# Optimization experiments

Measured on AMD Instinct MI355X. Metric: run time of the kernel, lower is better.

Reference implementation:

```python
import jax, jax.numpy as jnp
import numpy as np

NUM_HEADS = 4

def setup_inputs() -> dict:
    key = jax.random.key(0)
    ks = jax.random.split(key, 6)
    B, C, D, H, W = 2, 64, 16, 16, 16
    return {
        "x": jax.random.normal(ks[0], (B, C, D, H, W), dtype=jnp.float32),
        "tpm": jax.random.uniform(ks[1], (B, 1, D, H, W), dtype=jnp.float32),
        "qkv_w": jax.random.normal(ks[2], (3 * C, C), dtype=jnp.float32) * 0.05,
        "qkv_b": jax.random.normal(ks[3], (3 * C,), dtype=jnp.float32) * 0.02,
        "proj_w": jax.random.normal(ks[4], (C, C), dtype=jnp.float32) * 0.05,
        "proj_b": jax.random.normal(ks[5], (C,), dtype=jnp.float32) * 0.02,
        "temperature": jnp.ones((1,), dtype=jnp.float32),
    }


def reference(x, tpm, qkv_w, qkv_b, proj_w, proj_b, temperature):
    B, C, D, H, W = x.shape
    N = D * H * W
    nh = NUM_HEADS
    hd = C // nh
    scale = hd ** (-0.5)

    xf = x.reshape(B, C, N)
    # 1x1x1 Conv3d == per-voxel linear over channels
    qkv = jnp.einsum('oc,bcn->bon', qkv_w, xf) + qkv_b[:, None]  # (B,3C,N)
    qkv = qkv.reshape(B, 3, nh, hd, N)
    q, k, v = qkv[:, 0], qkv[:, 1], qkv[:, 2]  # each (B,nh,hd,N)

    temp = jnp.clip(temperature, 0.1, 2.0)[0]
    attn = jnp.einsum('bhdi,bhdj->bhij', q, k) * (scale * temp)  # (B,nh,N,N)

    tpm_c = jnp.clip(tpm, 0.01, 1.0).reshape(B, 1, N)
    tpm_inter = (tpm_c[:, :, :, None] + tpm_c[:, :, None, :]) * 0.5  # (B,1,N,N)
    attn = attn * tpm_inter
    attn = jax.nn.softmax(attn, axis=-1)  # dropout p=0.0 -> identity

    out = jnp.einsum('bhij,bhdj->bhdi', attn, v)  # (B,nh,hd,N)
    out = out.reshape(B, C, N)
    out = jnp.einsum('oc,bcn->bon', proj_w, out) + proj_b[:, None]
    return out.reshape(B, C, D, H, W)
```

## Files before the change

### kernel.cpp

```cpp
#include <hip/hip_runtime.h>
#include <hip/hip_bf16.h>
#include <math.h>

typedef __attribute__((ext_vector_type(8))) short bf16x8_t;
typedef __attribute__((ext_vector_type(4))) int i32x4_t;
typedef __attribute__((ext_vector_type(2))) int i32x2_t;
typedef __attribute__((ext_vector_type(4))) float f32x4_t;
typedef __attribute__((ext_vector_type(16))) float f32x16_t;

#define NH 4
#define HD 16
#define NN 4096
#define CC 64

__device__ __forceinline__ short f2bf(float f) {
  union { float f; unsigned u; } v; v.f = f;
  unsigned r = v.u + 0x7FFFu + ((v.u >> 16) & 1u);
  return (short)(r >> 16);
}

__global__ __launch_bounds__(256) void qkv_kernel(
    const float* __restrict__ x, const float* __restrict__ tpm,
    const float* __restrict__ qkv_w, const float* __restrict__ qkv_b,
    const float* __restrict__ temperature,
    short* __restrict__ Q, short* __restrict__ K, short* __restrict__ Kp,
    short* __restrict__ V, float* __restrict__ ts, short* __restrict__ ones) {
  __shared__ float xs[64][64];
  int bid = blockIdx.x;
  if (bid < 17) {
    int idx = bid * 256 + threadIdx.x;
    if (idx < 4352) ones[idx] = (short)0x3F80;
  }
  int nt = bid % 64;
  int which = (bid / 64) % 3;
  int b = bid / 192;
  int t = threadIdx.x;
  int nl = t & 63;
  int h = __builtin_amdgcn_readfirstlane(t >> 6);
  int n0 = nt * 64;
  int n = n0 + nl;

  {
    int c0 = t >> 6;
    const float* xb = x + ((size_t)b * 64) * NN + n0;
#pragma unroll
    for (int k = 0; k < 16; ++k) {
      int c = c0 + 4 * k;
      xs[c][nl] = xb[(size_t)c * NN + nl];
    }
  }
  __syncthreads();

  int obase = which * 64 + h * 16;
  float acc[16];
#pragma unroll
  for (int d = 0; d < 16; ++d) acc[d] = qkv_b[obase + d];

#pragma unroll 1
  for (int cb = 0; cb < 64; cb += 8) {
    float xr[8];
#pragma unroll
    for (int cc = 0; cc < 8; ++cc) xr[cc] = xs[cb + cc][nl];
#pragma unroll
    for (int d = 0; d < 16; ++d) {
#pragma unroll
      for (int cc = 0; cc < 8; ++cc)
        acc[d] += qkv_w[(obase + d) * 64 + cb + cc] * xr[cc];
    }
  }

  if (which == 2) {
#pragma unroll
    for (int d = 0; d < 16; ++d)
      V[(((size_t)b * NH + h) * HD + d) * NN + n] = f2bf(acc[d]);
    if (h == 0) {
      float tc = temperature[0];
      tc = fminf(fmaxf(tc, 0.1f), 2.0f);
      float tp = tpm[(size_t)b * NN + n];
      tp = fminf(fmaxf(tp, 0.01f), 1.0f);
      ts[(size_t)b * NN + n] = 0.125f * tc * tp * 1.44269504088896341f;
    }
  } else if (which == 0) {
    short pk[16];
#pragma unroll
    for (int d = 0; d < 16; ++d) pk[d] = f2bf(acc[d]);
    short* dst = Q + (((size_t)b * NH + h) * NN + n) * HD;
    *(bf16x8_t*)dst = *(bf16x8_t*)&pk[0];
    *(bf16x8_t*)(dst + 8) = *(bf16x8_t*)&pk[8];
  } else {
    float tc = temperature[0];
    tc = fminf(fmaxf(tc, 0.1f), 2.0f);
    float tp = tpm[(size_t)b * NN + n];
    tp = fminf(fmaxf(tp, 0.01f), 1.0f);
    float tsn = 0.125f * tc * tp * 1.44269504088896341f;
    short pk[16], pkp[16];
#pragma unroll
    for (int d = 0; d < 16; ++d) { pk[d] = f2bf(acc[d]); pkp[d] = f2bf(acc[d] * tsn); }
    short* dst = K + (((size_t)b * NH + h) * NN + n) * HD;
    *(bf16x8_t*)dst = *(bf16x8_t*)&pk[0];
    *(bf16x8_t*)(dst + 8) = *(bf16x8_t*)&pk[8];
    short* dstp = Kp + (((size_t)b * NH + h) * NN + n) * HD;
    *(bf16x8_t*)dstp = *(bf16x8_t*)&pkp[0];
    *(bf16x8_t*)(dstp + 8) = *(bf16x8_t*)&pkp[8];
  }
}

__global__ __launch_bounds__(256, 4) void attn_kernel(
    const short* __restrict__ Q, const short* __restrict__ K, const short* __restrict__ Kp,
    const short* __restrict__ V, const short* __restrict__ ones, const float* __restrict__ ts,
    float* __restrict__ OP, float* __restrict__ LP, int jcount) {
  int bid = blockIdx.x;
  int tile = bid & 31;
  int bh = (bid >> 5) & 7;
  int seg = bid >> 8;
  int b = bh >> 2, h = bh & 3;

  int tid = threadIdx.x;
  int w = tid >> 6;
  int lane = tid & 63;
  int half = lane >> 5;
  int l31 = lane & 31;

  int qi0 = tile * 128 + w * 32;
  const short* Qb = Q + (((size_t)b * NH + h) * NN) * HD;
  const short* Kb = K + (((size_t)b * NH + h) * NN) * HD;
  const short* Kpb = Kp + (((size_t)b * NH + h) * NN) * HD;
  const short* Vb = V + (((size_t)b * NH + h) * HD) * NN;

  float tsi = ts[(size_t)b * NN + qi0 + l31];
  bf16x8_t qf = *(const bf16x8_t*)(Qb + (size_t)(qi0 + l31) * HD + 8 * half);

  int jbase = seg * jcount;
  const short* vrow = (l31 < 16) ? (Vb + (size_t)l31 * NN + jbase) : ones;

  f32x16_t acc = {0.f,0.f,0.f,0.f,0.f,0.f,0.f,0.f,0.f,0.f,0.f,0.f,0.f,0.f,0.f,0.f};
  const f32x16_t z16 = {0.f,0.f,0.f,0.f,0.f,0.f,0.f,0.f,0.f,0.f,0.f,0.f,0.f,0.f,0.f,0.f};

#pragma unroll 4
  for (int jj = 0; jj < jcount; jj += 32) {
    const short* kptr = Kb + (size_t)(jbase + jj + l31) * HD + 8 * half;
    const short* kpptr = Kpb + (size_t)(jbase + jj + l31) * HD + 8 * half;
    bf16x8_t ak = *(const bf16x8_t*)kptr;
    bf16x8_t akp = *(const bf16x8_t*)kpptr;
    f32x16_t s = __builtin_amdgcn_mfma_f32_32x32x16_bf16(ak, qf, z16, 0, 0, 0);
    f32x16_t sp = __builtin_amdgcn_mfma_f32_32x32x16_bf16(akp, qf, z16, 0, 0, 0);

    float p[16];
#pragma unroll
    for (int r = 0; r < 16; ++r)
      p[r] = __builtin_amdgcn_exp2f(s[r] * tsi + sp[r]);

    int wr[8];
#pragma unroll
    for (int m = 0; m < 8; ++m)
      asm("v_cvt_pk_bf16_f32 %0, %1, %2" : "=v"(wr[m]) : "v"(p[2 * m]), "v"(p[2 * m + 1]));

    i32x2_t s02 = __builtin_amdgcn_permlane32_swap(wr[0], wr[2], false, false);
    i32x2_t s13 = __builtin_amdgcn_permlane32_swap(wr[1], wr[3], false, false);
    i32x2_t s46 = __builtin_amdgcn_permlane32_swap(wr[4], wr[6], false, false);
    i32x2_t s57 = __builtin_amdgcn_permlane32_swap(wr[5], wr[7], false, false);
    union { i32x4_t i; bf16x8_t b; } pa0, pa1;
    pa0.i = (i32x4_t){s02[0], s13[0], s02[1], s13[1]};
    pa1.i = (i32x4_t){s46[0], s57[0], s46[1], s57[1]};

    bf16x8_t bv0 = *(const bf16x8_t*)(vrow + jj + 8 * half);
    bf16x8_t bv1 = *(const bf16x8_t*)(vrow + jj + 16 + 8 * half);
    acc = __builtin_amdgcn_mfma_f32_32x32x16_bf16(pa0.b, bv0, acc, 0, 0, 0);
    acc = __builtin_amdgcn_mfma_f32_32x32x16_bf16(pa1.b, bv1, acc, 0, 0, 0);
  }

  float* OPb = OP + ((((size_t)seg * 2 + b) * NH + h) * HD) * NN;
  float* LPb = LP + (((size_t)seg * 2 + b) * NH + h) * NN;
  if (l31 < 16) {
#pragma unroll
    for (int g4 = 0; g4 < 4; ++g4) {
      f32x4_t vv = {acc[4 * g4 + 0], acc[4 * g4 + 1], acc[4 * g4 + 2], acc[4 * g4 + 3]};
      *(f32x4_t*)(OPb + (size_t)l31 * NN + qi0 + 4 * half + 8 * g4) = vv;
    }
  } else if (l31 == 16) {
#pragma unroll
    for (int g4 = 0; g4 < 4; ++g4) {
      f32x4_t vv = {acc[4 * g4 + 0], acc[4 * g4 + 1], acc[4 * g4 + 2], acc[4 * g4 + 3]};
      *(f32x4_t*)(LPb + qi0 + 4 * half + 8 * g4) = vv;
    }
  }
}

template <int SK>
__global__ __launch_bounds__(256) void proj_kernel_t(
    const float* __restrict__ OP, const float* __restrict__ LP,
    const float* __restrict__ proj_w, const float* __restrict__ proj_b,
    float* __restrict__ out) {
  __shared__ float pv[64][32];
  int bid = blockIdx.x;
  int b = bid >> 7;
  int n0 = (bid & 127) << 5;
  int t = threadIdx.x;
  int nl = t & 31;
  int g = t >> 5;
  int n = n0 + nl;
  int h = g >> 1;

  float lpv[SK];
#pragma unroll
  for (int s = 0; s < SK; ++s)
    lpv[s] = LP[(((size_t)s * 2 + b) * NH + h) * NN + n];
  float opv[8][SK];
#pragma unroll
  for (int cc = 0; cc < 8; ++cc) {
    int d = (g * 8 + cc) & 15;
#pragma unroll
    for (int s = 0; s < SK; ++s)
      opv[cc][s] = OP[((((size_t)s * 2 + b) * NH + h) * HD + d) * NN + n];
  }
  float ls = 0.f;
#pragma unroll
  for (int s = 0; s < SK; ++s) ls += lpv[s];
  float inv = 1.0f / ls;
#pragma unroll
  for (int cc = 0; cc < 8; ++cc) {
    float a = 0.f;
#pragma unroll
    for (int s = 0; s < SK; ++s) a += opv[cc][s];
    pv[g * 8 + cc][nl] = a * inv;
  }
  __syncthreads();

#pragma unroll
  for (int oo = 0; oo < 8; ++oo) {
    int o = g * 8 + oo;
    float a = proj_b[o];
#pragma unroll
    for (int c = 0; c < 64; ++c) a += proj_w[o * 64 + c] * pv[c][nl];
    out[((size_t)b * CC + o) * NN + n] = a;
  }
}

extern "C" void kernel_launch(void* const* d_in, const int* in_sizes, int n_in,
                              void* d_out, int out_size, void* d_ws, size_t ws_size,
                              hipStream_t stream) {
  const float* x = (const float*)d_in[0];
  const float* tpm = (const float*)d_in[1];
  const float* qkv_w = (const float*)d_in[2];
  const float* qkv_b = (const float*)d_in[3];
  const float* proj_w = (const float*)d_in[4];
  const float* proj_b = (const float*)d_in[5];
  const float* temperature = (const float*)d_in[6];
  float* out = (float*)d_out;

  const size_t MB = 1u << 20;
  char* ws = (char*)d_ws;
  short* Q    = (short*)(ws);
  short* K    = (short*)(ws + 1 * MB);
  short* Kp   = (short*)(ws + 2 * MB);
  short* V    = (short*)(ws + 3 * MB);
  float* ts   = (float*)(ws + 4 * MB);
  short* ones = (short*)(ws + 4 * MB + 32768);
  size_t lp_off = 4 * MB + 49152;

  int SK = 1;
  for (int cand = 4; cand >= 1; cand >>= 1) {
    size_t need = lp_off + (size_t)cand * (128 * 1024) + (size_t)cand * (2 * MB);
    if (ws_size >= need) { SK = cand; break; }
  }
  float* LP = (float*)(ws + lp_off);
  float* OP = (float*)(ws + lp_off + (size_t)SK * 128 * 1024);

  qkv_kernel<<<2 * 3 * 64, 256, 0, stream>>>(x, tpm, qkv_w, qkv_b, temperature, Q, K, Kp, V, ts, ones);
  attn_kernel<<<SK * 256, 256, 0, stream>>>(Q, K, Kp, V, ones, ts, OP, LP, NN / SK);
  if (SK == 4)      proj_kernel_t<4><<<2 * 128, 256, 0, stream>>>(OP, LP, proj_w, proj_b, out);
  else if (SK == 2) proj_kernel_t<2><<<2 * 128, 256, 0, stream>>>(OP, LP, proj_w, proj_b, out);
  else              proj_kernel_t<1><<<2 * 128, 256, 0, stream>>>(OP, LP, proj_w, proj_b, out);
}
```

Baseline: 61.90 us.

## Rework attention inner loop around 16x16x32 MFMA with explicit row sums

The attention kernel moves from 32x32x16 MFMAs over 32-query tiles to 16x16x32 MFMAs over 16-query tiles per wave. The old version needed cross-half permlane swaps and a ones-row padded into V to get the softmax denominator. The new one computes the score and scaled-score products by zero-padding the B operand, sums exp values in registers and reduces them with shuffles. The ones buffer and its init are dropped, the grid doubles, the occupancy hint goes from 4 to 8 and the loop count is a template constant. This trades some wasted MFMA work from the zero padding for less data shuffling and more parallelism.

After: 102.1 us. +65.0%, slower.

```diff
diff --git a/kernel.cpp b/kernel.cpp
--- a/kernel.cpp
+++ b/kernel.cpp
@@ -3,10 +3,9 @@
 #include <math.h>
 
 typedef __attribute__((ext_vector_type(8))) short bf16x8_t;
+typedef __attribute__((ext_vector_type(4))) short short4_t;
 typedef __attribute__((ext_vector_type(4))) int i32x4_t;
-typedef __attribute__((ext_vector_type(2))) int i32x2_t;
 typedef __attribute__((ext_vector_type(4))) float f32x4_t;
-typedef __attribute__((ext_vector_type(16))) float f32x16_t;
 
 #define NH 4
 #define HD 16
@@ -24,13 +23,9 @@
     const float* __restrict__ qkv_w, const float* __restrict__ qkv_b,
     const float* __restrict__ temperature,
     short* __restrict__ Q, short* __restrict__ K, short* __restrict__ Kp,
-    short* __restrict__ V, float* __restrict__ ts, short* __restrict__ ones) {
+    short* __restrict__ V, float* __restrict__ ts) {
   __shared__ float xs[64][64];
   int bid = blockIdx.x;
-  if (bid < 17) {
-    int idx = bid * 256 + threadIdx.x;
-    if (idx < 4352) ones[idx] = (short)0x3F80;
-  }
   int nt = bid % 64;
   int which = (bid / 64) % 3;
   int b = bid / 192;
@@ -105,85 +100,83 @@
   }
 }
 
-__global__ __launch_bounds__(256, 4) void attn_kernel(
+template <int JC>
+__global__ __launch_bounds__(256, 8) void attn_kernel_t(
     const short* __restrict__ Q, const short* __restrict__ K, const short* __restrict__ Kp,
-    const short* __restrict__ V, const short* __restrict__ ones, const float* __restrict__ ts,
-    float* __restrict__ OP, float* __restrict__ LP, int jcount) {
+    const short* __restrict__ V, const float* __restrict__ ts,
+    float* __restrict__ OP, float* __restrict__ LP) {
   int bid = blockIdx.x;
-  int tile = bid & 31;
-  int bh = (bid >> 5) & 7;
-  int seg = bid >> 8;
+  int tile = bid & 63;
+  int bh = (bid >> 6) & 7;
+  int seg = bid >> 9;
   int b = bh >> 2, h = bh & 3;
 
   int tid = threadIdx.x;
   int w = tid >> 6;
   int lane = tid & 63;
-  int half = lane >> 5;
-  int l31 = lane & 31;
-
-  int qi0 = tile * 128 + w * 32;
-  const short* Qb = Q + (((size_t)b * NH + h) * NN) * HD;
-  const short* Kb = K + (((size_t)b * NH + h) * NN) * HD;
+  int c = lane & 15;
+  int g = lane >> 4;
+
+  int qi0 = tile * 64 + w * 16;
+  const short* Qb  = Q  + (((size_t)b * NH + h) * NN) * HD;
+  const short* Kb  = K  + (((size_t)b * NH + h) * NN) * HD;
   const short* Kpb = Kp + (((size_t)b * NH + h) * NN) * HD;
-  const short* Vb = V + (((size_t)b * NH + h) * HD) * NN;
-
-  float tsi = ts[(size_t)b * NN + qi0 + l31];
-  bf16x8_t qf = *(const bf16x8_t*)(Qb + (size_t)(qi0 + l31) * HD + 8 * half);
-
-  int jbase = seg * jcount;
-  const short* vrow = (l31 < 16) ? (Vb + (size_t)l31 * NN + jbase) : ones;
-
-  f32x16_t acc = {0.f,0.f,0.f,0.f,0.f,0.f,0.f,0.f,0.f,0.f,0.f,0.f,0.f,0.f,0.f,0.f};
-  const f32x16_t z16 = {0.f,0.f,0.f,0.f,0.f,0.f,0.f,0.f,0.f,0.f,0.f,0.f,0.f,0.f,0.f,0.f};
-
-#pragma unroll 4
-  for (int jj = 0; jj < jcount; jj += 32) {
-    const short* kptr = Kb + (size_t)(jbase + jj + l31) * HD + 8 * half;
-    const short* kpptr = Kpb + (size_t)(jbase + jj + l31) * HD + 8 * half;
-    bf16x8_t ak = *(const bf16x8_t*)kptr;
-    bf16x8_t akp = *(const bf16x8_t*)kpptr;
-    f32x16_t s = __builtin_amdgcn_mfma_f32_32x32x16_bf16(ak, qf, z16, 0, 0, 0);
-    f32x16_t sp = __builtin_amdgcn_mfma_f32_32x32x16_bf16(akp, qf, z16, 0, 0, 0);
-
-    float p[16];
-#pragma unroll
-    for (int r = 0; r < 16; ++r)
-      p[r] = __builtin_amdgcn_exp2f(s[r] * tsi + sp[r]);
-
-    int wr[8];
-#pragma unroll
-    for (int m = 0; m < 8; ++m)
-      asm("v_cvt_pk_bf16_f32 %0, %1, %2" : "=v"(wr[m]) : "v"(p[2 * m]), "v"(p[2 * m + 1]));
-
-    i32x2_t s02 = __builtin_amdgcn_permlane32_swap(wr[0], wr[2], false, false);
-    i32x2_t s13 = __builtin_amdgcn_permlane32_swap(wr[1], wr[3], false, false);
-    i32x2_t s46 = __builtin_amdgcn_permlane32_swap(wr[4], wr[6], false, false);
-    i32x2_t s57 = __builtin_amdgcn_permlane32_swap(wr[5], wr[7], false, false);
-    union { i32x4_t i; bf16x8_t b; } pa0, pa1;
-    pa0.i = (i32x4_t){s02[0], s13[0], s02[1], s13[1]};
-    pa1.i = (i32x4_t){s46[0], s57[0], s46[1], s57[1]};
-
-    bf16x8_t bv0 = *(const bf16x8_t*)(vrow + jj + 8 * half);
-    bf16x8_t bv1 = *(const bf16x8_t*)(vrow + jj + 16 + 8 * half);
-    acc = __builtin_amdgcn_mfma_f32_32x32x16_bf16(pa0.b, bv0, acc, 0, 0, 0);
-    acc = __builtin_amdgcn_mfma_f32_32x32x16_bf16(pa1.b, bv1, acc, 0, 0, 0);
-  }
+  const short* Vb  = V  + (((size_t)b * NH + h) * HD) * NN;
+
+  float tsi = ts[(size_t)b * NN + qi0 + c];
+
+  bf16x8_t qv = *(const bf16x8_t*)(Qb + (size_t)(qi0 + c) * HD + (g & 1) * 8);
+  bf16x8_t zero8 = {0, 0, 0, 0, 0, 0, 0, 0};
+  bf16x8_t Bs, Bsp;
+  if (g < 2) { Bs = qv; Bsp = zero8; } else { Bs = zero8; Bsp = qv; }
+
+  int jbase = seg * JC;
+  const short* kbase = ((g < 2) ? Kb : Kpb) + (size_t)(jbase + c) * HD + (g & 1) * 8;
+  const short* vbase = Vb + (size_t)c * NN + jbase + 4 * g;
+
+  f32x4_t acc = {0.f, 0.f, 0.f, 0.f};
+  float dsum = 0.f;
+  const f32x4_t z4 = {0.f, 0.f, 0.f, 0.f};
+
+#pragma unroll 1
+  for (int jj = 0; jj < JC; jj += 32) {
+    bf16x8_t a0 = *(const bf16x8_t*)(kbase + (size_t)jj * HD);
+    bf16x8_t a1 = *(const bf16x8_t*)(kbase + (size_t)(jj + 16) * HD);
+    f32x4_t s0  = __builtin_amdgcn_mfma_f32_16x16x32_bf16(a0, Bs,  z4, 0, 0, 0);
+    f32x4_t sp0 = __builtin_amdgcn_mfma_f32_16x16x32_bf16(a0, Bsp, z4, 0, 0, 0);
+    f32x4_t s1  = __builtin_amdgcn_mfma_f32_16x16x32_bf16(a1, Bs,  z4, 0, 0, 0);
+    f32x4_t sp1 = __builtin_amdgcn_mfma_f32_16x16x32_bf16(a1, Bsp, z4, 0, 0, 0);
+
+    float p0[4], p1[4];
+#pragma unroll
+    for (int r = 0; r < 4; ++r) {
+      p0[r] = __builtin_amdgcn_exp2f(fmaf(s0[r], tsi, sp0[r]));
+      p1[r] = __builtin_amdgcn_exp2f(fmaf(s1[r], tsi, sp1[r]));
+      dsum += p0[r] + p1[r];
+    }
+
+    int w0, w1, w2, w3;
+    asm("v_cvt_pk_bf16_f32 %0, %1, %2" : "=v"(w0) : "v"(p0[0]), "v"(p0[1]));
+    asm("v_cvt_pk_bf16_f32 %0, %1, %2" : "=v"(w1) : "v"(p0[2]), "v"(p0[3]));
+    asm("v_cvt_pk_bf16_f32 %0, %1, %2" : "=v"(w2) : "v"(p1[0]), "v"(p1[1]));
+    asm("v_cvt_pk_bf16_f32 %0, %1, %2" : "=v"(w3) : "v"(p1[2]), "v"(p1[3]));
+    union { i32x4_t i; bf16x8_t b; } A2;
+    A2.i = (i32x4_t){w0, w1, w2, w3};
+
+    union { short4_t s[2]; bf16x8_t b; } B2;
+    B2.s[0] = *(const short4_t*)(vbase + jj);
+    B2.s[1] = *(const short4_t*)(vbase + jj + 16);
+
+    acc = __builtin_amdgcn_mfma_f32_16x16x32_bf16(A2.b, B2.b, acc, 0, 0, 0);
+  }
+
+  dsum += __shfl_xor(dsum, 16);
+  dsum += __shfl_xor(dsum, 32);
 
   float* OPb = OP + ((((size_t)seg * 2 + b) * NH + h) * HD) * NN;
   float* LPb = LP + (((size_t)seg * 2 + b) * NH + h) * NN;
-  if (l31 < 16) {
-#pragma unroll
-    for (int g4 = 0; g4 < 4; ++g4) {
-      f32x4_t vv = {acc[4 * g4 + 0], acc[4 * g4 + 1], acc[4 * g4 + 2], acc[4 * g4 + 3]};
-      *(f32x4_t*)(OPb + (size_t)l31 * NN + qi0 + 4 * half + 8 * g4) = vv;
-    }
-  } else if (l31 == 16) {
-#pragma unroll
-    for (int g4 = 0; g4 < 4; ++g4) {
-      f32x4_t vv = {acc[4 * g4 + 0], acc[4 * g4 + 1], acc[4 * g4 + 2], acc[4 * g4 + 3]};
-      *(f32x4_t*)(LPb + qi0 + 4 * half + 8 * g4) = vv;
-    }
-  }
+  *(f32x4_t*)(OPb + (size_t)c * NN + qi0 + 4 * g) = acc;
+  if (g == 0) LPb[qi0 + c] = dsum;
 }
 
 template <int SK>
@@ -250,13 +243,12 @@
 
   const size_t MB = 1u << 20;
   char* ws = (char*)d_ws;
-  short* Q    = (short*)(ws);
-  short* K    = (short*)(ws + 1 * MB);
-  short* Kp   = (short*)(ws + 2 * MB);
-  short* V    = (short*)(ws + 3 * MB);
-  float* ts   = (float*)(ws + 4 * MB);
-  short* ones = (short*)(ws + 4 * MB + 32768);
-  size_t lp_off = 4 * MB + 49152;
+  short* Q  = (short*)(ws);
+  short* K  = (short*)(ws + 1 * MB);
+  short* Kp = (short*)(ws + 2 * MB);
+  short* V  = (short*)(ws + 3 * MB);
+  float* ts = (float*)(ws + 4 * MB);
+  size_t lp_off = 4 * MB + 32768;
 
   int SK = 1;
   for (int cand = 4; cand >= 1; cand >>= 1) {
@@ -266,8 +258,10 @@
   float* LP = (float*)(ws + lp_off);
   float* OP = (float*)(ws + lp_off + (size_t)SK * 128 * 1024);
 
-  qkv_kernel<<<2 * 3 * 64, 256, 0, stream>>>(x, tpm, qkv_w, qkv_b, temperature, Q, K, Kp, V, ts, ones);
-  attn_kernel<<<SK * 256, 256, 0, stream>>>(Q, K, Kp, V, ones, ts, OP, LP, NN / SK);
+  qkv_kernel<<<2 * 3 * 64, 256, 0, stream>>>(x, tpm, qkv_w, qkv_b, temperature, Q, K, Kp, V, ts);
+  if (SK == 4)      attn_kernel_t<1024><<<4 * 512, 256, 0, stream>>>(Q, K, Kp, V, ts, OP, LP);
+  else if (SK == 2) attn_kernel_t<2048><<<2 * 512, 256, 0, stream>>>(Q, K, Kp, V, ts, OP, LP);
+  else              attn_kernel_t<4096><<<1 * 512, 256, 0, stream>>>(Q, K, Kp, V, ts, OP, LP);
   if (SK == 4)      proj_kernel_t<4><<<2 * 128, 256, 0, stream>>>(OP, LP, proj_w, proj_b, out);
   else if (SK == 2) proj_kernel_t<2><<<2 * 128, 256, 0, stream>>>(OP, LP, proj_w, proj_b, out);
   else              proj_kernel_t<1><<<2 * 128, 256, 0, stream>>>(OP, LP, proj_w, proj_b, out);
```
